# Kernel tuning notes

Measured on AMD Instinct MI355X. Metric: run time of the kernel, lower is better.

The kernel has to match this reference:

```python
import jax, jax.numpy as jnp
import numpy as np


def setup_inputs() -> dict:
    key = jax.random.key(0)
    B, L, D, N = 2, 2048, 1024, 16
    ks = jax.random.split(key, 8)
    s = 1.0 / np.sqrt(D)
    # S4D-real init for A_log, matching the module
    A_log = jnp.log(jnp.broadcast_to(jnp.arange(1, N + 1, dtype=jnp.float32), (D, N)))
    return {
        "x": jax.random.normal(ks[0], (B, L, D), jnp.float32),
        "Wz": jax.random.normal(ks[1], (D, D), jnp.float32) * s,
        "bz": jnp.zeros((D,), jnp.float32),
        "Wx": jax.random.normal(ks[2], (D, D), jnp.float32) * s,
        "bx": jnp.zeros((D,), jnp.float32),
        "WB": jax.random.normal(ks[3], (D, N), jnp.float32) * s,
        "bB": jnp.zeros((N,), jnp.float32),
        "WC": jax.random.normal(ks[4], (D, N), jnp.float32) * s,
        "bC": jnp.zeros((N,), jnp.float32),
        "Wdt": jax.random.normal(ks[5], (D, D), jnp.float32) * s,
        "bdt": jnp.zeros((D,), jnp.float32),
        "A_log": A_log,
        "Wout": jax.random.normal(ks[6], (D, D), jnp.float32) * s,
        "bout": jnp.zeros((D,), jnp.float32),
    }


def reference(x, Wz, bz, Wx, bx, WB, bB, WC, bC, Wdt, bdt, A_log, Wout, bout):
    B, L, D = x.shape
    N = A_log.shape[1]

    # input-dependent projections
    z = jax.nn.sigmoid(x @ Wz + bz)            # (B,L,D) gate
    x_ssm = x @ Wx + bx                        # (B,L,D)
    Bm = x @ WB + bB                           # (B,L,N)
    C = x @ WC + bC                            # (B,L,N)
    dt = jax.nn.softplus(x @ Wdt + bdt)        # (B,L,D)

    A = -jnp.exp(A_log)                        # (D,N)
    A_bar = jnp.exp(dt[..., None] * A)         # (B,L,D,N) discretized state matrix
    # x_db = x_ssm * (dt * B)  -> (B,L,D,N)
    x_db = x_ssm[..., None] * (dt[..., None] * Bm[..., None, :])

    # scan over time: move L to leading axis
    a_scan = jnp.transpose(A_bar, (1, 0, 2, 3))   # (L,B,D,N)
    x_scan = jnp.transpose(x_db, (1, 0, 2, 3))    # (L,B,D,N)
    c_scan = jnp.transpose(C, (1, 0, 2))          # (L,B,N)

    def ssm_step(h, inp):
        a_t, x_t, c_t = inp                       # (B,D,N),(B,D,N),(B,N)
        h_new = a_t * h + x_t
        y_t = jnp.einsum('bdn,bn->bd', h_new, c_t)
        return h_new, y_t

    h0 = jnp.zeros((B, D, N), x.dtype)
    _, y_ssm = jax.lax.scan(ssm_step, h0, (a_scan, x_scan, c_scan))
    y_ssm = jnp.transpose(y_ssm, (1, 0, 2))       # (B,L,D)

    y = y_ssm * z
    return y @ Wout + bout
```

## Files before the change

kernel.cpp:

```cpp
#include <hip/hip_runtime.h>
#include <math.h>

#define CHUNKS 64
#define LCH    32

#define GBM 128
#define GBN 128
#define GBK 32

typedef __attribute__((ext_vector_type(8))) short bf16x8;
typedef __attribute__((ext_vector_type(4))) float f32x4;
typedef __attribute__((ext_vector_type(8))) unsigned short us8;
typedef __attribute__((ext_vector_type(4))) unsigned short us4;

typedef __attribute__((address_space(1))) const unsigned int gu32;
typedef __attribute__((address_space(3))) unsigned int lu32;

__device__ __forceinline__ void gload16(const unsigned short* g, unsigned short* l) {
    __builtin_amdgcn_global_load_lds((gu32*)g, (lu32*)l, 16, 0, 0);
}

__device__ __forceinline__ unsigned short f2bf(float f) {
    unsigned int u = __float_as_uint(f);
    unsigned int r = (u + 0x7FFFu + ((u >> 16) & 1u)) >> 16;
    return (unsigned short)r;
}

__global__ __launch_bounds__(256) void convert_bf16(
    const float* __restrict__ in, unsigned short* __restrict__ out, int n4)
{
    int i = blockIdx.x * 256 + threadIdx.x;
    if (i < n4) {
        float4 v = ((const float4*)in)[i];
        us4 u;
        u[0] = f2bf(v.x); u[1] = f2bf(v.y); u[2] = f2bf(v.z); u[3] = f2bf(v.w);
        ((us4*)out)[i] = u;
    }
}

__global__ __launch_bounds__(256) void transpose4_bf16(
    const float* __restrict__ W0, const float* __restrict__ W1,
    const float* __restrict__ W2, const float* __restrict__ W3,
    unsigned short* __restrict__ T0, unsigned short* __restrict__ T1,
    unsigned short* __restrict__ T2, unsigned short* __restrict__ T3, int D)
{
    const float* W = (blockIdx.z == 0) ? W0 : (blockIdx.z == 1) ? W1
                   : (blockIdx.z == 2) ? W2 : W3;
    unsigned short* Wt = (blockIdx.z == 0) ? T0 : (blockIdx.z == 1) ? T1
                       : (blockIdx.z == 2) ? T2 : T3;

    __shared__ float Ls[64][65];
    const int n0 = blockIdx.x * 64;
    const int k0 = blockIdx.y * 64;
    const int tx = threadIdx.x;

#pragma unroll
    for (int i = 0; i < 4; i++) {
        int idx = tx + i * 256;
        int kr = idx >> 4;
        int ng = idx & 15;
        float4 v = *(const float4*)&W[(size_t)(k0 + kr) * D + n0 + ng * 4];
        Ls[kr][ng * 4 + 0] = v.x;
        Ls[kr][ng * 4 + 1] = v.y;
        Ls[kr][ng * 4 + 2] = v.z;
        Ls[kr][ng * 4 + 3] = v.w;
    }
    __syncthreads();
#pragma unroll
    for (int i = 0; i < 4; i++) {
        int idx = tx + i * 256;
        int nr = idx >> 4;
        int kg = idx & 15;
        us4 u;
#pragma unroll
        for (int j = 0; j < 4; j++) u[j] = f2bf(Ls[kg * 4 + j][nr]);
        *(us4*)&Wt[(size_t)(n0 + nr) * D + k0 + kg * 4] = u;
    }
}

__device__ __forceinline__ void stage_tile(
    const unsigned short* __restrict__ A, const unsigned short* __restrict__ B,
    unsigned short* As, unsigned short* Bs,
    int brow, int bcol, int K, int k0, int wave, int srow, int sq)
{
    gload16(&A[(size_t)(brow + wave * 32      + srow) * K + k0 + sq],
            &As[(wave * 32) * GBK]);
    gload16(&A[(size_t)(brow + wave * 32 + 16 + srow) * K + k0 + sq],
            &As[(wave * 32 + 16) * GBK]);
    gload16(&B[(size_t)(bcol + wave * 32      + srow) * K + k0 + sq],
            &Bs[(wave * 32) * GBK]);
    gload16(&B[(size_t)(bcol + wave * 32 + 16 + srow) * K + k0 + sq],
            &Bs[(wave * 32 + 16) * GBK]);
}

__device__ __forceinline__ void gemm_core(
    const unsigned short* __restrict__ A, const unsigned short* __restrict__ B,
    unsigned short* As, unsigned short* Bs,
    int brow, int bcol, int K, f32x4 acc[4][4],
    int wave, int lane, int wr, int wc, int lrow, int lk)
{
    const int srow = lane >> 2;
    const int sq   = ((lane & 3) ^ ((lane >> 3) & 3)) * 8;

#pragma unroll
    for (int m = 0; m < 4; m++)
#pragma unroll
        for (int n = 0; n < 4; n++) acc[m][n] = (f32x4)(0.f);

    stage_tile(A, B, As, Bs, brow, bcol, K, 0, wave, srow, sq);
    asm volatile("s_waitcnt vmcnt(0)" ::: "memory");
    __builtin_amdgcn_s_barrier();

    int cur = 0;
    for (int k0 = 0; k0 < K; k0 += GBK) {
        if (k0 + GBK < K) {
            stage_tile(A, B, As + (cur ^ 1) * (GBM * GBK), Bs + (cur ^ 1) * (GBN * GBK),
                       brow, bcol, K, k0 + GBK, wave, srow, sq);
            asm volatile("s_waitcnt vmcnt(4)" ::: "memory");
        } else {
            asm volatile("s_waitcnt vmcnt(0)" ::: "memory");
        }
        __builtin_amdgcn_s_barrier();

        const unsigned short* as = As + cur * (GBM * GBK);
        const unsigned short* bs = Bs + cur * (GBN * GBK);

        bf16x8 av[4], bv[4];
#pragma unroll
        for (int m = 0; m < 4; m++) {
            int row = wr * 64 + m * 16 + lrow;
            av[m] = *(const bf16x8*)&as[row * GBK + ((lk ^ ((row >> 1) & 3)) * 8)];
        }
#pragma unroll
        for (int n = 0; n < 4; n++) {
            int row = wc * 64 + n * 16 + lrow;
            bv[n] = *(const bf16x8*)&bs[row * GBK + ((lk ^ ((row >> 1) & 3)) * 8)];
        }
#pragma unroll
        for (int m = 0; m < 4; m++)
#pragma unroll
            for (int n = 0; n < 4; n++)
                acc[m][n] = __builtin_amdgcn_mfma_f32_16x16x32_bf16(
                    av[m], bv[n], acc[m][n], 0, 0, 0);

        asm volatile("s_waitcnt lgkmcnt(0)" ::: "memory");
        __builtin_amdgcn_s_barrier();
        cur ^= 1;
    }
}

__global__ __launch_bounds__(256) void proj3_gemm(
    const unsigned short* __restrict__ A,
    const unsigned short* __restrict__ W0, const unsigned short* __restrict__ W1,
    const unsigned short* __restrict__ W2,
    const float* __restrict__ b0, const float* __restrict__ b1,
    const float* __restrict__ b2,
    float* __restrict__ o0, float* __restrict__ o1, float* __restrict__ o2,
    int K, int Nc)
{
    __shared__ unsigned short As[2 * GBM * GBK];
    __shared__ unsigned short Bs[2 * GBN * GBK];

    const int widx = blockIdx.x >> 3;
    const unsigned short* B = (widx == 0) ? W0 : (widx == 1) ? W1 : W2;
    const float* bias = (widx == 0) ? b0 : (widx == 1) ? b1 : b2;
    float* out = (widx == 0) ? o0 : (widx == 1) ? o1 : o2;

    const int tx = threadIdx.x;
    const int wave = tx >> 6;
    const int lane = tx & 63;
    const int wr = wave >> 1, wc = wave & 1;
    const int lrow = lane & 15, lk = lane >> 4;
    const int brow = blockIdx.y * GBM;
    const int bcol = (blockIdx.x & 7) * GBN;

    f32x4 acc[4][4];
    gemm_core(A, B, As, Bs, brow, bcol, K, acc, wave, lane, wr, wc, lrow, lk);

#pragma unroll
    for (int n = 0; n < 4; n++) {
        int col = bcol + wc * 64 + n * 16 + lrow;
        float bval = bias[col];
#pragma unroll
        for (int m = 0; m < 4; m++) {
#pragma unroll
            for (int r = 0; r < 4; r++) {
                int row = brow + wr * 64 + m * 16 + lk * 4 + r;
                float v = acc[m][n][r] + bval;
                if (widx == 0) v = 1.f / (1.f + __expf(-v));
                else if (widx == 2) v = (v > 20.f) ? v : log1pf(__expf(v));
                out[(size_t)row * Nc + col] = v;
            }
        }
    }
}

__global__ __launch_bounds__(256) void gemm_bt(
    const unsigned short* __restrict__ A, const unsigned short* __restrict__ B,
    const float* __restrict__ bias, float* __restrict__ out, int K, int ldo)
{
    __shared__ unsigned short As[2 * GBM * GBK];
    __shared__ unsigned short Bs[2 * GBN * GBK];

    const int tx = threadIdx.x;
    const int wave = tx >> 6;
    const int lane = tx & 63;
    const int wr = wave >> 1, wc = wave & 1;
    const int lrow = lane & 15, lk = lane >> 4;
    const int brow = blockIdx.y * GBM;
    const int bcol = blockIdx.x * GBN;

    f32x4 acc[4][4];
    gemm_core(A, B, As, Bs, brow, bcol, K, acc, wave, lane, wr, wc, lrow, lk);

#pragma unroll
    for (int n = 0; n < 4; n++) {
        int col = bcol + wc * 64 + n * 16 + lrow;
        float bval = bias[col];
#pragma unroll
        for (int m = 0; m < 4; m++) {
#pragma unroll
            for (int r = 0; r < 4; r++) {
                int row = brow + wr * 64 + m * 16 + lk * 4 + r;
                out[(size_t)row * ldo + col] = acc[m][n][r] + bval;
            }
        }
    }
}

__global__ __launch_bounds__(256) void bc_proj(
    const float* __restrict__ x,
    const float* __restrict__ WB, const float* __restrict__ bB,
    const float* __restrict__ WC, const float* __restrict__ bC,
    float* __restrict__ BC, int K, int M)
{
    __shared__ unsigned short Wl[32 * 1024];

    const int tx = threadIdx.x;

#pragma unroll
    for (int i = 0; i < 16; i++) {
        int e = tx + i * 256;
        int k = e >> 2;
        int n0 = (e & 3) * 4;
        float4 v = ((const float4*)WB)[e];
        float vv[4] = {v.x, v.y, v.z, v.w};
#pragma unroll
        for (int j = 0; j < 4; j++) {
            int n = n0 + j;
            Wl[n * 1024 + (((k & ~7) ^ ((n & 15) << 3)) | (k & 7))] = f2bf(vv[j]);
        }
    }
#pragma unroll
    for (int i = 0; i < 16; i++) {
        int e = tx + i * 256;
        int k = e >> 2;
        int n0 = (e & 3) * 4;
        float4 v = ((const float4*)WC)[e];
        float vv[4] = {v.x, v.y, v.z, v.w};
#pragma unroll
        for (int j = 0; j < 4; j++) {
            int n = 16 + n0 + j;
            Wl[n * 1024 + (((k & ~7) ^ ((n & 15) << 3)) | (k & 7))] = f2bf(vv[j]);
        }
    }
    __syncthreads();

    const int n = tx & 31;
    const int r = tx >> 5;
    const int row = blockIdx.x * 8 + r;

    const unsigned short* wrow = &Wl[n * 1024];
    const int sw = (n & 15) << 3;
    const float* xrow = &x[(size_t)row * K];

    float acc = 0.f;
    for (int kb = 0; kb < K; kb += 8) {
        us8 w8 = *(const us8*)&wrow[kb ^ sw];
        float4 xa = *(const float4*)&xrow[kb];
        float4 xb = *(const float4*)&xrow[kb + 4];
        float xv[8] = {xa.x, xa.y, xa.z, xa.w, xb.x, xb.y, xb.z, xb.w};
#pragma unroll
        for (int j = 0; j < 8; j++) {
            acc = fmaf(xv[j], __uint_as_float((unsigned)(unsigned short)w8[j] << 16), acc);
        }
    }

    float bias = (n < 16) ? bB[n] : bC[n - 16];
    BC[(size_t)row * 32 + n] = acc + bias;
}

__global__ __launch_bounds__(256) void scan_phase1(
    const float* __restrict__ xs, const float* __restrict__ dt,
    const float* __restrict__ BC, const float* __restrict__ A_log,
    float* __restrict__ P, float* __restrict__ Hl, int L, int D, int M)
{
    const int tx = threadIdx.x;
    const int d  = blockIdx.x * 256 + tx;
    const int c  = blockIdx.y;
    const int b  = blockIdx.z;
    const int m0 = b * L + c * LCH;

    __shared__ float bcs[LCH][32];
    {
        int row = tx >> 3, col = (tx & 7) * 4;
        *(f32x4*)&bcs[row][col] = *(const f32x4*)&BC[(size_t)(m0 + row) * 32 + col];
    }
    __syncthreads();

    float Av[16];
#pragma unroll
    for (int i = 0; i < 4; i++) {
        f32x4 a4 = *(const f32x4*)&A_log[d * 16 + i * 4];
#pragma unroll
        for (int j = 0; j < 4; j++) Av[i * 4 + j] = -__expf(a4[j]);
    }

    float h[16];
#pragma unroll
    for (int n = 0; n < 16; n++) h[n] = 0.f;
    float dts = 0.f;

    const size_t base = (size_t)m0 * D + d;
    float dtv = dt[base], xv = xs[base];
    for (int t = 0; t < LCH; t++) {
        float dtn = 0.f, xvn = 0.f;
        if (t + 1 < LCH) {
            dtn = dt[base + (size_t)(t + 1) * D];
            xvn = xs[base + (size_t)(t + 1) * D];
        }
        float xdt = xv * dtv;
        dts += dtv;
        f32x4 bm[4];
#pragma unroll
        for (int i = 0; i < 4; i++) bm[i] = *(const f32x4*)&bcs[t][i * 4];
#pragma unroll
        for (int n = 0; n < 16; n++) {
            float a = __expf(dtv * Av[n]);
            h[n] = fmaf(a, h[n], xdt * bm[n >> 2][n & 3]);
        }
        dtv = dtn; xv = xvn;
    }

    size_t idx = (((size_t)b * D + d) * CHUNKS + c) * 16;
#pragma unroll
    for (int i = 0; i < 4; i++) {
        f32x4 p4, h4;
#pragma unroll
        for (int j = 0; j < 4; j++) {
            p4[j] = __expf(Av[i * 4 + j] * dts);
            h4[j] = h[i * 4 + j];
        }
        *(f32x4*)&P[idx + i * 4]  = p4;
        *(f32x4*)&Hl[idx + i * 4] = h4;
    }
}

__global__ __launch_bounds__(256) void scan_phase2(
    const float* __restrict__ P, float* __restrict__ Hl, int D, int N)
{
    const int tid = blockIdx.x * 256 + threadIdx.x;
    const int n = tid & 15;
    const int dd = (tid >> 4) & 1023;
    const int b = tid >> 14;

    size_t base = (((size_t)b * D + dd) * CHUNKS) * 16 + n;
    float run = 0.f;
#pragma unroll 4
    for (int c = 0; c < CHUNKS; c++) {
        float p   = P[base + (size_t)c * 16];
        float tmp = Hl[base + (size_t)c * 16];
        Hl[base + (size_t)c * 16] = run;
        run = fmaf(p, run, tmp);
    }
}

__global__ __launch_bounds__(256) void scan_phase3(
    const float* __restrict__ xs, const float* __restrict__ dt,
    const float* __restrict__ BC, const float* __restrict__ z,
    const float* __restrict__ A_log, const float* __restrict__ Hin,
    unsigned short* __restrict__ ybf, int L, int D, int M)
{
    const int tx = threadIdx.x;
    const int d  = blockIdx.x * 256 + tx;
    const int c  = blockIdx.y;
    const int b  = blockIdx.z;
    const int m0 = b * L + c * LCH;

    __shared__ float bcs[LCH][32];
    {
        int row = tx >> 3, col = (tx & 7) * 4;
        *(f32x4*)&bcs[row][col] = *(const f32x4*)&BC[(size_t)(m0 + row) * 32 + col];
    }
    __syncthreads();

    float Av[16];
#pragma unroll
    for (int i = 0; i < 4; i++) {
        f32x4 a4 = *(const f32x4*)&A_log[d * 16 + i * 4];
#pragma unroll
        for (int j = 0; j < 4; j++) Av[i * 4 + j] = -__expf(a4[j]);
    }

    float h[16];
    {
        size_t hidx = (((size_t)b * D + d) * CHUNKS + c) * 16;
#pragma unroll
        for (int i = 0; i < 4; i++) {
            f32x4 h4 = *(const f32x4*)&Hin[hidx + i * 4];
#pragma unroll
            for (int j = 0; j < 4; j++) h[i * 4 + j] = h4[j];
        }
    }

    const size_t base = (size_t)m0 * D + d;
    float dtv = dt[base], xv = xs[base], zv = z[base];
    for (int t = 0; t < LCH; t++) {
        float dtn = 0.f, xvn = 0.f, zvn = 0.f;
        if (t + 1 < LCH) {
            dtn = dt[base + (size_t)(t + 1) * D];
            xvn = xs[base + (size_t)(t + 1) * D];
            zvn = z[base + (size_t)(t + 1) * D];
        }
        float xdt = xv * dtv;
        f32x4 bm[4], cm[4];
#pragma unroll
        for (int i = 0; i < 4; i++) {
            bm[i] = *(const f32x4*)&bcs[t][i * 4];
            cm[i] = *(const f32x4*)&bcs[t][16 + i * 4];
        }
        float y = 0.f;
#pragma unroll
        for (int n = 0; n < 16; n++) {
            float a = __expf(dtv * Av[n]);
            h[n] = fmaf(a, h[n], xdt * bm[n >> 2][n & 3]);
            y = fmaf(h[n], cm[n >> 2][n & 3], y);
        }
        ybf[base + (size_t)t * D] = f2bf(y * zv);
        dtv = dtn; xv = xvn; zv = zvn;
    }
}

extern "C" void kernel_launch(void* const* d_in, const int* in_sizes, int n_in,
                              void* d_out, int out_size, void* d_ws, size_t ws_size,
                              hipStream_t stream) {
    const float* x     = (const float*)d_in[0];
    const float* Wz    = (const float*)d_in[1];
    const float* bz    = (const float*)d_in[2];
    const float* Wx    = (const float*)d_in[3];
    const float* bx    = (const float*)d_in[4];
    const float* WB    = (const float*)d_in[5];
    const float* bB    = (const float*)d_in[6];
    const float* WC    = (const float*)d_in[7];
    const float* bC    = (const float*)d_in[8];
    const float* Wdt   = (const float*)d_in[9];
    const float* bdt   = (const float*)d_in[10];
    const float* A_log = (const float*)d_in[11];
    const float* Wout  = (const float*)d_in[12];
    const float* bout  = (const float*)d_in[13];
    float* out = (float*)d_out;

    const int Bb = 2, L = 2048, D = 1024, N = 16;
    const int M = Bb * L;
    const size_t MD = (size_t)M * D;

    float* ws   = (float*)d_ws;
    float* xsb  = ws;
    float* dtb  = xsb + MD;
    float* BCb  = dtb + MD;
    float* Pb   = BCb + (size_t)M * 32;
    float* Hlb  = Pb  + (size_t)Bb * D * CHUNKS * 16;
    unsigned short* xbf   = (unsigned short*)(Hlb + (size_t)Bb * D * CHUNKS * 16);
    unsigned short* Wzt   = xbf + MD;
    unsigned short* Wxt   = Wzt + (size_t)D * D;
    unsigned short* Wdtt  = Wxt + (size_t)D * D;
    unsigned short* Woutt = Wdtt + (size_t)D * D;
    float* zb = out;

    dim3 blk(256);
    dim3 gridT(D / 64, D / 64, 4);

    convert_bf16<<<dim3((unsigned)(MD / 4 / 256)), blk, 0, stream>>>(x, xbf, (int)(MD / 4));
    transpose4_bf16<<<gridT, blk, 0, stream>>>(Wz, Wx, Wdt, Wout,
                                               Wzt, Wxt, Wdtt, Woutt, D);

    proj3_gemm<<<dim3(3 * D / GBN, M / GBM), blk, 0, stream>>>(
        xbf, Wzt, Wxt, Wdtt, bz, bx, bdt, zb, xsb, dtb, D, D);
    bc_proj<<<dim3(M / 8), blk, 0, stream>>>(x, WB, bB, WC, bC, BCb, D, M);

    dim3 gridScan(D / 256, CHUNKS, Bb);
    scan_phase1<<<gridScan, blk, 0, stream>>>(xsb, dtb, BCb, A_log, Pb, Hlb, L, D, M);
    scan_phase2<<<dim3(Bb * D * N / 256), blk, 0, stream>>>(Pb, Hlb, D, N);
    scan_phase3<<<gridScan, blk, 0, stream>>>(xsb, dtb, BCb, zb, A_log, Hlb,
                                              xbf , L, D, M);

    gemm_bt<<<dim3(D / GBN, M / GBM), blk, 0, stream>>>(xbf, Woutt, bout, out, D, D);
}
```

Measured before the change: 169.5 us.

## Triple-buffer GEMM tile loads and remap blocks for XCD-aware L2 locality

The GEMM core moves from double to triple buffering in LDS, keeping two tile loads in flight with adjusted vmcnt waits to hide global latency. Both GEMM kernels now launch a 1D grid and remap block IDs so blocks that share row panels land on the same XCD (bid&7), aiming to improve L2 reuse. The cost is 50% more LDS per block, which may reduce occupancy.

```diff
diff --git a/kernel.cpp b/kernel.cpp
--- a/kernel.cpp
+++ b/kernel.cpp
@@ -7,6 +7,8 @@
 #define GBM 128
 #define GBN 128
 #define GBK 32
+#define ATILE (GBM * GBK)
+#define BTILE (GBN * GBK)
 
 typedef __attribute__((ext_vector_type(8))) short bf16x8;
 typedef __attribute__((ext_vector_type(4))) float f32x4;
@@ -107,23 +109,26 @@
 #pragma unroll
         for (int n = 0; n < 4; n++) acc[m][n] = (f32x4)(0.f);
 
-    stage_tile(A, B, As, Bs, brow, bcol, K, 0, wave, srow, sq);
-    asm volatile("s_waitcnt vmcnt(0)" ::: "memory");
-    __builtin_amdgcn_s_barrier();
+    const int nk = K / GBK;
+    stage_tile(A, B, As,         Bs,         brow, bcol, K, 0,   wave, srow, sq);
+    stage_tile(A, B, As + ATILE, Bs + BTILE, brow, bcol, K, GBK, wave, srow, sq);
 
     int cur = 0;
-    for (int k0 = 0; k0 < K; k0 += GBK) {
-        if (k0 + GBK < K) {
-            stage_tile(A, B, As + (cur ^ 1) * (GBM * GBK), Bs + (cur ^ 1) * (GBN * GBK),
-                       brow, bcol, K, k0 + GBK, wave, srow, sq);
+    int nxt = 2;
+    for (int kt = 0; kt < nk; ++kt) {
+        if (kt + 2 < nk) {
+            stage_tile(A, B, As + nxt * ATILE, Bs + nxt * BTILE,
+                       brow, bcol, K, (kt + 2) * GBK, wave, srow, sq);
+            asm volatile("s_waitcnt vmcnt(8)" ::: "memory");
+        } else if (kt + 1 < nk) {
             asm volatile("s_waitcnt vmcnt(4)" ::: "memory");
         } else {
             asm volatile("s_waitcnt vmcnt(0)" ::: "memory");
         }
         __builtin_amdgcn_s_barrier();
 
-        const unsigned short* as = As + cur * (GBM * GBK);
-        const unsigned short* bs = Bs + cur * (GBN * GBK);
+        const unsigned short* as = As + cur * ATILE;
+        const unsigned short* bs = Bs + cur * BTILE;
 
         bf16x8 av[4], bv[4];
 #pragma unroll
@@ -145,7 +150,8 @@
 
         asm volatile("s_waitcnt lgkmcnt(0)" ::: "memory");
         __builtin_amdgcn_s_barrier();
-        cur ^= 1;
+        cur = (cur == 2) ? 0 : cur + 1;
+        nxt = (nxt == 2) ? 0 : nxt + 1;
     }
 }
 
@@ -158,10 +164,15 @@
     float* __restrict__ o0, float* __restrict__ o1, float* __restrict__ o2,
     int K, int Nc)
 {
-    __shared__ unsigned short As[2 * GBM * GBK];
-    __shared__ unsigned short Bs[2 * GBN * GBK];
-
-    const int widx = blockIdx.x >> 3;
+    __shared__ unsigned short As[3 * ATILE];
+    __shared__ unsigned short Bs[3 * BTILE];
+
+    const int bid = blockIdx.x;
+    const int idx = bid >> 3;
+    const int by  = (bid & 7) * 4 + idx / 24;
+    const int bx  = idx % 24;
+
+    const int widx = bx >> 3;
     const unsigned short* B = (widx == 0) ? W0 : (widx == 1) ? W1 : W2;
     const float* bias = (widx == 0) ? b0 : (widx == 1) ? b1 : b2;
     float* out = (widx == 0) ? o0 : (widx == 1) ? o1 : o2;
@@ -171,8 +182,8 @@
     const int lane = tx & 63;
     const int wr = wave >> 1, wc = wave & 1;
     const int lrow = lane & 15, lk = lane >> 4;
-    const int brow = blockIdx.y * GBM;
-    const int bcol = (blockIdx.x & 7) * GBN;
+    const int brow = by * GBM;
+    const int bcol = (bx & 7) * GBN;
 
     f32x4 acc[4][4];
     gemm_core(A, B, As, Bs, brow, bcol, K, acc, wave, lane, wr, wc, lrow, lk);
@@ -199,16 +210,21 @@
     const unsigned short* __restrict__ A, const unsigned short* __restrict__ B,
     const float* __restrict__ bias, float* __restrict__ out, int K, int ldo)
 {
-    __shared__ unsigned short As[2 * GBM * GBK];
-    __shared__ unsigned short Bs[2 * GBN * GBK];
+    __shared__ unsigned short As[3 * ATILE];
+    __shared__ unsigned short Bs[3 * BTILE];
+
+    const int bid = blockIdx.x;
+    const int idx = bid >> 3;
+    const int by  = (bid & 7) * 4 + idx / 8;
+    const int bx  = idx % 8;
 
     const int tx = threadIdx.x;
     const int wave = tx >> 6;
     const int lane = tx & 63;
     const int wr = wave >> 1, wc = wave & 1;
     const int lrow = lane & 15, lk = lane >> 4;
-    const int brow = blockIdx.y * GBM;
-    const int bcol = blockIdx.x * GBN;
+    const int brow = by * GBM;
+    const int bcol = bx * GBN;
 
     f32x4 acc[4][4];
     gemm_core(A, B, As, Bs, brow, bcol, K, acc, wave, lane, wr, wc, lrow, lk);
@@ -484,7 +500,7 @@
     transpose4_bf16<<<gridT, blk, 0, stream>>>(Wz, Wx, Wdt, Wout,
                                                Wzt, Wxt, Wdtt, Woutt, D);
 
-    proj3_gemm<<<dim3(3 * D / GBN, M / GBM), blk, 0, stream>>>(
+    proj3_gemm<<<dim3(3 * (D / GBN) * (M / GBM)), blk, 0, stream>>>(
         xbf, Wzt, Wxt, Wdtt, bz, bx, bdt, zb, xsb, dtb, D, D);
     bc_proj<<<dim3(M / 8), blk, 0, stream>>>(x, WB, bB, WC, bC, BCb, D, M);
 
@@ -494,5 +510,5 @@
     scan_phase3<<<gridScan, blk, 0, stream>>>(xsb, dtb, BCb, zb, A_log, Hlb,
                                               xbf , L, D, M);
 
-    gemm_bt<<<dim3(D / GBN, M / GBM), blk, 0, stream>>>(xbf, Woutt, bout, out, D, D);
-}
+    gemm_bt<<<dim3((D / GBN) * (M / GBM)), blk, 0, stream>>>(xbf, Woutt, bout, out, D, D);
+}
```

After: 166.6 us. Within noise of the previous version (-1.7%).
